# Kernel tuning notes

Measured on AMD Instinct MI355X. Metric: run time of the kernel, lower is better.

Reference implementation:

```python
import jax, jax.numpy as jnp
import numpy as np


def _ens_linear(x, W, b):
    # x: [B,T,Din], W: [E,Din,Dout], b: [E,Dout] -> [E,B,T,Dout]
    return jnp.einsum('btd,edh->ebth', x, W) + b[:, None, None, :]


def _gilr_scan(v, f):
    # h_t = f_t * h_{t-1} + (1 - f_t) * v_t, h_0 = 0 (tie-input-gate linear recurrence)
    def comb(c1, c2):
        a1, b1 = c1
        a2, b2 = c2
        return a2 * a1, a2 * b1 + b2
    _, h = jax.lax.associative_scan(comb, (f, (1.0 - f) * v), axis=1)
    return h


def setup_inputs() -> dict:
    key = jax.random.key(0)
    ks = jax.random.split(key, 7)
    B, T, Din, D = 8, 4096, 512, 512
    x = jax.random.normal(ks[0], (B, T, Din), dtype=jnp.float32)
    s_in = 1.0 / np.sqrt(Din)
    s = 1.0 / np.sqrt(D)
    W_in = jax.random.uniform(ks[1], (2, Din, D), jnp.float32, -s_in, s_in)
    b_in = jax.random.uniform(ks[2], (2, D), jnp.float32, -s_in, s_in)
    W_mid = jax.random.uniform(ks[3], (4, D, D), jnp.float32, -s, s)
    b_mid = jax.random.uniform(ks[4], (4, D), jnp.float32, -s, s)
    W_out = jax.random.uniform(ks[5], (D, D), jnp.float32, -s, s)
    b_out = jax.random.uniform(ks[6], (D,), jnp.float32, -s, s)
    return {"x": x, "W_in": W_in, "b_in": b_in, "W_mid": W_mid,
            "b_mid": b_mid, "W_out": W_out, "b_out": b_out}


def reference(x, W_in, b_in, W_mid, b_mid, W_out, b_out):
    # in_proj (ensemble of 2): u[0] -> v, u[1] -> f
    u = _ens_linear(x, W_in, b_in)
    v = jnp.tanh(u[0])
    f = jax.nn.sigmoid(u[1])
    # first gated linear recurrence (hidden_pre starts at zeros)
    v = _gilr_scan(v, f)
    hidden_pre = v[:, -1:, :]
    # middle_proj (ensemble of 4): f, i, o, z
    u = _ens_linear(v, W_mid, b_mid)
    f2 = jax.nn.sigmoid(u[0])
    i = jax.nn.sigmoid(u[1])
    o = jax.nn.sigmoid(u[2])
    z = jnp.tanh(u[3])
    # second gated linear recurrence (hidden_middle starts at zeros)
    out = _gilr_scan(i * z, f2)
    hidden_middle = out[:, -1:, :]
    out = out * o
    out = out @ W_out + b_out
    hidden = jnp.concatenate((hidden_pre, hidden_middle), axis=-1)
    hidden = jnp.transpose(hidden, (1, 0, 2))  # [1, B, 2D]
    return out, hidden
```

## Files before the change

kernel.cpp:

```cpp
#include <hip/hip_runtime.h>

typedef short short8 __attribute__((ext_vector_type(8)));
typedef float float4v __attribute__((ext_vector_type(4)));
typedef unsigned short u16;
typedef unsigned int u32;

#define T_LEN 4096
#define DDIM 512
#define BATCH 8
#define MROWS 32768
#define CH 32
#define NC 128

__device__ __forceinline__ u16 f2b(float x) {
    unsigned u = __float_as_uint(x);
    unsigned r = (u + 0x7FFFu + ((u >> 16) & 1u)) >> 16;
    return (u16)r;
}
__device__ __forceinline__ float b2f(u16 h) {
    return __uint_as_float((u32)h << 16);
}
__device__ __forceinline__ float sigm(float x) {
    return __builtin_amdgcn_rcpf(1.f + __builtin_amdgcn_exp2f(-1.44269504f * x));
}
__device__ __forceinline__ float tanh_fast(float x) {
    return 1.f - 2.f * __builtin_amdgcn_rcpf(1.f + __builtin_amdgcn_exp2f(2.88539008f * x));
}

__device__ __forceinline__ void gl2lds16(const u16* g, u16* l) {
    __builtin_amdgcn_global_load_lds(
        (const __attribute__((address_space(1))) void*)g,
        (__attribute__((address_space(3))) void*)l, 16, 0, 0);
}

__device__ __forceinline__ void compose_xor(float& A, float& B, int mask,
                                            bool selfIsHi) {
    float pa = __shfl_xor(A, mask);
    float pb = __shfl_xor(B, mask);
    float loA = selfIsHi ? pa : A, loB = selfIsHi ? pb : B;
    float hiA = selfIsHi ? A : pa, hiB = selfIsHi ? B : pb;
    A = hiA * loA;
    B = hiA * loB + hiB;
}

__global__ __launch_bounds__(256) void cvt_x(const float* __restrict__ x,
                                             u16* __restrict__ xb, size_t n) {
    size_t i = ((size_t)blockIdx.x * 256 + threadIdx.x) * 4;
    if (i < n) {
        float4v v = *(const float4v*)&x[i];
        ushort4 p;
        p.x = f2b(v[0]); p.y = f2b(v[1]); p.z = f2b(v[2]); p.w = f2b(v[3]);
        *(ushort4*)&xb[i] = p;
    }
}

template <int MODE>
__global__ __launch_bounds__(256) void cvt_wt(const float* __restrict__ W,
                                              u16* __restrict__ Wt, int N) {
    int idx = blockIdx.x * 256 + threadIdx.x;
    if (idx >= N * 512) return;
    int j = idx >> 9;
    int k = idx & 511;
    int gate, d;
    if (MODE == 1) { gate = (j >> 4) & 1; d = (j >> 5) * 16 + (j & 15); }
    else if (MODE == 2) { gate = (j >> 4) & 3; d = (j >> 6) * 16 + (j & 15); }
    else { gate = 0; d = j; }
    Wt[(size_t)j * 512 + k] = f2b(W[((size_t)gate * 512 + k) * 512 + d]);
}

template <int MODE>
__global__ __launch_bounds__(512, 4) void gemm_act(
    const u16* __restrict__ A, const u16* __restrict__ Bt,
    const float* __restrict__ bias, void* __restrict__ o0v,
    void* __restrict__ o1v, void* __restrict__ o2v,
    float* __restrict__ cA, float* __restrict__ cB) {
    constexpr int K = 512;
    constexpr int BK = 32;
    constexpr int NKT = K / BK;
    constexpr int LBA = 256 * 32;
    constexpr int LBB = 128 * 32;
    constexpr int GX = (MODE == 1) ? 8 : (MODE == 2) ? 16 : 4;
    constexpr int NWG = 128 * GX;
    __shared__ u16 lsA[3][LBA];
    __shared__ u16 lsB[3][LBB];
    const int tid = threadIdx.x;
    const int lane = tid & 63;
    const int wid = tid >> 6;
    const int wr = wid >> 1;
    const int wc = wid & 1;
    const int l0 = lane & 15, lh = lane >> 4;

    const int h = blockIdx.x;
    const int l = (h & 7) * (NWG / 8) + (h >> 3);
    const int bn0 = (l & (GX - 1)) * 128;
    const int bm0 = (l / GX) * 256;

    float4v acc[4][4];
#pragma unroll
    for (int m = 0; m < 4; ++m)
#pragma unroll
        for (int n = 0; n < 4; ++n) acc[m][n] = (float4v){0.f, 0.f, 0.f, 0.f};

    int growA[2], gchA[2], growB, gchB;
#pragma unroll
    for (int i = 0; i < 2; ++i) {
        int flat = i * 512 + tid;
        growA[i] = flat >> 2;
        gchA[i] = (((flat & 3) ^ ((growA[i] >> 1) & 3))) * 8;
    }
    growB = tid >> 2;
    gchB = (((tid & 3) ^ ((growB >> 1) & 3))) * 8;

#define STAGE(buf, kt)                                                        \
    {                                                                         \
        const int k0 = (kt) * BK;                                             \
        _Pragma("unroll") for (int i = 0; i < 2; ++i)                         \
            gl2lds16(&A[(size_t)(bm0 + growA[i]) * K + k0 + gchA[i]],         \
                     &lsA[buf][(i * 512 + tid) * 8]);                         \
        gl2lds16(&Bt[(size_t)(bn0 + growB) * K + k0 + gchB],                  \
                 &lsB[buf][tid * 8]);                                         \
    }

    STAGE(0, 0);
    STAGE(1, 1);

    for (int kt = 0; kt < NKT; ++kt) {
        const int cur = kt % 3;
        if (kt + 1 < NKT)
            asm volatile("s_waitcnt vmcnt(3)" ::: "memory");
        else
            asm volatile("s_waitcnt vmcnt(0)" ::: "memory");
        __builtin_amdgcn_s_barrier();
        __builtin_amdgcn_sched_barrier(0);
        if (kt + 2 < NKT) STAGE((kt + 2) % 3, kt + 2);
        short8 af[4], bf[4];
#pragma unroll
        for (int m = 0; m < 4; ++m) {
            int r = wr * 64 + m * 16 + l0;
            af[m] = *(const short8*)&lsA[cur][r * 32 + ((lh ^ ((r >> 1) & 3)) * 8)];
        }
#pragma unroll
        for (int n = 0; n < 4; ++n) {
            int r = wc * 64 + n * 16 + l0;
            bf[n] = *(const short8*)&lsB[cur][r * 32 + ((lh ^ ((r >> 1) & 3)) * 8)];
        }
        asm volatile("s_waitcnt lgkmcnt(0)" ::: "memory");
        __builtin_amdgcn_sched_barrier(0);
        __builtin_amdgcn_s_setprio(1);
#pragma unroll
        for (int m = 0; m < 4; ++m)
#pragma unroll
            for (int n = 0; n < 4; ++n)
                acc[m][n] = __builtin_amdgcn_mfma_f32_16x16x32_bf16(
                    af[m], bf[n], acc[m][n], 0, 0, 0);
        __builtin_amdgcn_s_setprio(0);
    }
#undef STAGE

    if (MODE == 3) {
#pragma unroll
        for (int m = 0; m < 4; ++m) {
#pragma unroll
            for (int n = 0; n < 4; ++n) {
                int col = bn0 + wc * 64 + n * 16 + l0;
                float bv = bias[col];
#pragma unroll
                for (int r = 0; r < 4; ++r) {
                    int rw = bm0 + wr * 64 + m * 16 + lh * 4 + r;
                    ((float*)o0v)[(size_t)rw * 512 + col] = acc[m][n][r] + bv;
                }
            }
        }
        return;
    }

    const int bb = bm0 >> 12;
    const int tq = (bm0 & 4095) + wr * 64;

    if (MODE == 1) {
        const int base5 = (bn0 + wc * 64) >> 5;
#pragma unroll
        for (int p = 0; p < 2; ++p) {
            const int d = (base5 + p) * 16 + l0;
            const float bvv = bias[d], bvf = bias[512 + d];
            float segA[4], segB[4];
#pragma unroll
            for (int m = 0; m < 4; ++m) {
                float Ap = 1.f, Bp = 0.f;
#pragma unroll
                for (int r = 0; r < 4; ++r) {
                    int rw = bm0 + wr * 64 + m * 16 + lh * 4 + r;
                    float f1 = sigm(acc[m][2 * p + 1][r] + bvf);
                    float g = (1.f - f1) * tanh_fast(acc[m][2 * p][r] + bvv);
                    size_t oidx = (size_t)rw * 512 + d;
                    ((u16*)o0v)[oidx] = f2b(f1);
                    ((u16*)o1v)[oidx] = f2b(g);
                    Bp = f1 * Bp + g;
                    Ap *= f1;
                }
                segA[m] = Ap; segB[m] = Bp;
            }
#pragma unroll
            for (int m = 0; m < 4; ++m) {
                compose_xor(segA[m], segB[m], 16, (lh & 1) != 0);
                compose_xor(segA[m], segB[m], 32, (lh & 2) != 0);
            }
            if (lh == 0) {
                float c0A = segA[1] * segA[0], c0B = segA[1] * segB[0] + segB[1];
                float c1A = segA[3] * segA[2], c1B = segA[3] * segB[2] + segB[3];
                int c0 = tq >> 5;
                size_t ci0 = (size_t)c0 * 4096 + bb * 512 + d;
                size_t ci1 = ci0 + 4096;
                cA[ci0] = c0A; cB[ci0] = c0B;
                cA[ci1] = c1A; cB[ci1] = c1B;
            }
        }
    } else {
        const int d = ((bn0 + wc * 64) >> 6) * 16 + l0;
        const float bv0 = bias[d], bv1 = bias[512 + d];
        const float bv2 = bias[1024 + d], bv3 = bias[1536 + d];
        float segA[4], segB[4];
#pragma unroll
        for (int m = 0; m < 4; ++m) {
            float Ap = 1.f, Bp = 0.f;
#pragma unroll
            for (int r = 0; r < 4; ++r) {
                int rw = bm0 + wr * 64 + m * 16 + lh * 4 + r;
                float f2 = sigm(acc[m][0][r] + bv0);
                float ii = sigm(acc[m][1][r] + bv1);
                float oo = sigm(acc[m][2][r] + bv2);
                float zz = tanh_fast(acc[m][3][r] + bv3);
                float g = (1.f - f2) * ii * zz;
                size_t oidx = (size_t)rw * 512 + d;
                ((u16*)o0v)[oidx] = f2b(f2);
                ((u16*)o1v)[oidx] = f2b(g);
                ((u16*)o2v)[oidx] = f2b(oo);
                Bp = f2 * Bp + g;
                Ap *= f2;
            }
            segA[m] = Ap; segB[m] = Bp;
        }
#pragma unroll
        for (int m = 0; m < 4; ++m) {
            compose_xor(segA[m], segB[m], 16, (lh & 1) != 0);
            compose_xor(segA[m], segB[m], 32, (lh & 2) != 0);
        }
        if (lh == 0) {
            float c0A = segA[1] * segA[0], c0B = segA[1] * segB[0] + segB[1];
            float c1A = segA[3] * segA[2], c1B = segA[3] * segB[2] + segB[3];
            int c0 = tq >> 5;
            size_t ci0 = (size_t)c0 * 4096 + bb * 512 + d;
            size_t ci1 = ci0 + 4096;
            cA[ci0] = c0A; cB[ci0] = c0B;
            cA[ci1] = c1A; cB[ci1] = c1B;
        }
    }
}

__global__ __launch_bounds__(256) void scan_p2(float* __restrict__ cA,
                                               const float* __restrict__ cB) {
    int ln = blockIdx.x * 256 + threadIdx.x;
    float h = 0.f;
    for (int c = 0; c < NC; ++c) {
        size_t ix = (size_t)c * 4096 + ln;
        float a = cA[ix], bb = cB[ix];
        cA[ix] = h;
        h = a * h + bb;
    }
}

template <int S>
__global__ __launch_bounds__(128) void scan_p3(
    const u16* __restrict__ f, const u16* __restrict__ g,
    const u16* __restrict__ o, const float* __restrict__ cA,
    u16* __restrict__ hb, float* __restrict__ hid) {
    int d0 = threadIdx.x * 4;
    int c = blockIdx.x & (NC - 1);
    int b = blockIdx.x >> 7;
    size_t base = ((size_t)b * T_LEN + c * CH) * DDIM + d0;
    size_t ci = (size_t)c * 4096 + b * DDIM + d0;
    float h[4] = {cA[ci], cA[ci + 1], cA[ci + 2], cA[ci + 3]};
    for (int t = 0; t < CH; ++t) {
        ushort4 fq = *(const ushort4*)&f[base];
        ushort4 gq = *(const ushort4*)&g[base];
        float ff[4] = {b2f(fq.x), b2f(fq.y), b2f(fq.z), b2f(fq.w)};
        float gg[4] = {b2f(gq.x), b2f(gq.y), b2f(gq.z), b2f(gq.w)};
        float w[4];
#pragma unroll
        for (int j = 0; j < 4; ++j) {
            h[j] = ff[j] * h[j] + gg[j];
            w[j] = h[j];
        }
        if (S == 2) {
            ushort4 oq = *(const ushort4*)&o[base];
            w[0] *= b2f(oq.x); w[1] *= b2f(oq.y);
            w[2] *= b2f(oq.z); w[3] *= b2f(oq.w);
        }
        ushort4 p;
        p.x = f2b(w[0]); p.y = f2b(w[1]); p.z = f2b(w[2]); p.w = f2b(w[3]);
        *(ushort4*)&hb[base] = p;
        base += DDIM;
    }
    if (c == NC - 1) {
#pragma unroll
        for (int j = 0; j < 4; ++j)
            hid[b * 1024 + (S == 1 ? 0 : 512) + d0 + j] = h[j];
    }
}

extern "C" void kernel_launch(void* const* d_in, const int* in_sizes, int n_in,
                              void* d_out, int out_size, void* d_ws,
                              size_t ws_size, hipStream_t stream) {
    const float* x = (const float*)d_in[0];
    const float* W_in = (const float*)d_in[1];
    const float* b_in = (const float*)d_in[2];
    const float* W_mid = (const float*)d_in[3];
    const float* b_mid = (const float*)d_in[4];
    const float* W_out = (const float*)d_in[5];
    const float* b_out = (const float*)d_in[6];
    float* out = (float*)d_out;
    char* ws = (char*)d_ws;

    const size_t MB = 1u << 20;
    const size_t MD = (size_t)MROWS * DDIM;

    u16* wt_in = (u16*)(ws);
    u16* wt_mid = (u16*)(ws + 1 * MB);
    u16* wt_out = (u16*)(ws + 3 * MB);
    u16* hb = (u16*)(ws + 4 * MB);
    u16* S0 = (u16*)(ws + 36 * MB);
    u16* S1 = (u16*)(ws + 68 * MB);
    u16* S2 = (u16*)(ws + 100 * MB);
    float* cA = (float*)(ws + 164 * MB);
    float* cB = (float*)(ws + 166 * MB);
    float* hid = out + MD;

    cvt_x<<<(int)(MD / 4 / 256), 256, 0, stream>>>(x, hb, MD);
    cvt_wt<1><<<(1024 * 512) / 256, 256, 0, stream>>>(W_in, wt_in, 1024);
    cvt_wt<2><<<(2048 * 512) / 256, 256, 0, stream>>>(W_mid, wt_mid, 2048);
    cvt_wt<3><<<(512 * 512) / 256, 256, 0, stream>>>(W_out, wt_out, 512);

    gemm_act<1><<<1024, 512, 0, stream>>>(hb, wt_in, b_in, S0, S1, nullptr,
                                          cA, cB);
    scan_p2<<<16, 256, 0, stream>>>(cA, cB);
    scan_p3<1><<<1024, 128, 0, stream>>>(S0, S1, nullptr, cA, hb, hid);

    gemm_act<2><<<2048, 512, 0, stream>>>(hb, wt_mid, b_mid, S0, S1, S2,
                                          cA, cB);
    scan_p2<<<16, 256, 0, stream>>>(cA, cB);
    scan_p3<2><<<1024, 128, 0, stream>>>(S0, S1, S2, cA, hb, hid);

    gemm_act<3><<<512, 512, 0, stream>>>(hb, wt_out, b_out, out, nullptr,
                                         nullptr, nullptr, nullptr);
}
```

Before: 244.0 us.

## Fuse fp32-to-bf16 input conversion into first GEMM and merge weight conversions

Removes the standalone cvt_x pass. The first GEMM now reads fp32 x directly, converts it to bf16 in registers and writes it into swizzled LDS, using a double-buffered register-prefetch pipeline with __syncthreads. The three weight-conversion launches are merged into one kernel. This saves a full read/write pass over x and two launches, but the MODE 1 GEMM drops its async global_load_lds triple buffering for a simpler sync-based loop, which may reduce overlap.

```diff
diff --git a/kernel.cpp b/kernel.cpp
--- a/kernel.cpp
+++ b/kernel.cpp
@@ -2,6 +2,7 @@
 
 typedef short short8 __attribute__((ext_vector_type(8)));
 typedef float float4v __attribute__((ext_vector_type(4)));
+typedef int int4v __attribute__((ext_vector_type(4)));
 typedef unsigned short u16;
 typedef unsigned int u32;
 
@@ -16,6 +17,9 @@
     unsigned u = __float_as_uint(x);
     unsigned r = (u + 0x7FFFu + ((u >> 16) & 1u)) >> 16;
     return (u16)r;
+}
+__device__ __forceinline__ u32 pk2(float a, float b) {
+    return (u32)f2b(a) | ((u32)f2b(b) << 16);
 }
 __device__ __forceinline__ float b2f(u16 h) {
     return __uint_as_float((u32)h << 16);
@@ -43,34 +47,31 @@
     B = hiA * loB + hiB;
 }
 
-__global__ __launch_bounds__(256) void cvt_x(const float* __restrict__ x,
-                                             u16* __restrict__ xb, size_t n) {
-    size_t i = ((size_t)blockIdx.x * 256 + threadIdx.x) * 4;
-    if (i < n) {
-        float4v v = *(const float4v*)&x[i];
-        ushort4 p;
-        p.x = f2b(v[0]); p.y = f2b(v[1]); p.z = f2b(v[2]); p.w = f2b(v[3]);
-        *(ushort4*)&xb[i] = p;
-    }
-}
-
-template <int MODE>
-__global__ __launch_bounds__(256) void cvt_wt(const float* __restrict__ W,
-                                              u16* __restrict__ Wt, int N) {
+__global__ __launch_bounds__(256) void cvt_wt_all(
+    const float* __restrict__ W_in, const float* __restrict__ W_mid,
+    const float* __restrict__ W_out, u16* __restrict__ wt_in,
+    u16* __restrict__ wt_mid, u16* __restrict__ wt_out) {
     int idx = blockIdx.x * 256 + threadIdx.x;
-    if (idx >= N * 512) return;
     int j = idx >> 9;
     int k = idx & 511;
-    int gate, d;
-    if (MODE == 1) { gate = (j >> 4) & 1; d = (j >> 5) * 16 + (j & 15); }
-    else if (MODE == 2) { gate = (j >> 4) & 3; d = (j >> 6) * 16 + (j & 15); }
-    else { gate = 0; d = j; }
-    Wt[(size_t)j * 512 + k] = f2b(W[((size_t)gate * 512 + k) * 512 + d]);
+    if (j < 1024) {
+        int gate = (j >> 4) & 1, d = (j >> 5) * 16 + (j & 15);
+        wt_in[(size_t)j * 512 + k] =
+            f2b(W_in[((size_t)gate * 512 + k) * 512 + d]);
+    } else if (j < 3072) {
+        int j2 = j - 1024;
+        int gate = (j2 >> 4) & 3, d = (j2 >> 6) * 16 + (j2 & 15);
+        wt_mid[(size_t)j2 * 512 + k] =
+            f2b(W_mid[((size_t)gate * 512 + k) * 512 + d]);
+    } else {
+        int j3 = j - 3072;
+        wt_out[(size_t)j3 * 512 + k] = f2b(W_out[(size_t)k * 512 + j3]);
+    }
 }
 
 template <int MODE>
 __global__ __launch_bounds__(512, 4) void gemm_act(
-    const u16* __restrict__ A, const u16* __restrict__ Bt,
+    const void* __restrict__ Av, const u16* __restrict__ Bt,
     const float* __restrict__ bias, void* __restrict__ o0v,
     void* __restrict__ o1v, void* __restrict__ o2v,
     float* __restrict__ cA, float* __restrict__ cB) {
@@ -101,15 +102,83 @@
 #pragma unroll
         for (int n = 0; n < 4; ++n) acc[m][n] = (float4v){0.f, 0.f, 0.f, 0.f};
 
-    int growA[2], gchA[2], growB, gchB;
-#pragma unroll
-    for (int i = 0; i < 2; ++i) {
-        int flat = i * 512 + tid;
-        growA[i] = flat >> 2;
-        gchA[i] = (((flat & 3) ^ ((growA[i] >> 1) & 3))) * 8;
-    }
-    growB = tid >> 2;
-    gchB = (((tid & 3) ^ ((growB >> 1) & 3))) * 8;
+    const int growB = tid >> 2;
+    const int gchB = (((tid & 3) ^ ((growB >> 1) & 3))) * 8;
+
+    if constexpr (MODE == 1) {
+        const float* Af = (const float*)Av;
+        const int ar = tid >> 1, ah = tid & 1;
+        const float* agp = &Af[(size_t)(bm0 + ar) * 512 + ah * 16];
+        const int s3 = (ar >> 1) & 3;
+        u16* adst0 = &lsA[0][ar * 32 + (((2 * ah) ^ s3)) * 8];
+        u16* adst1 = &lsA[0][ar * 32 + (((2 * ah + 1) ^ s3)) * 8];
+
+#define CVTWRITE(buf, v0, v1, v2, v3)                                         \
+    {                                                                         \
+        int4v wA = {(int)pk2(v0[0], v0[1]), (int)pk2(v0[2], v0[3]),           \
+                    (int)pk2(v1[0], v1[1]), (int)pk2(v1[2], v1[3])};          \
+        int4v wB = {(int)pk2(v2[0], v2[1]), (int)pk2(v2[2], v2[3]),           \
+                    (int)pk2(v3[0], v3[1]), (int)pk2(v3[2], v3[3])};          \
+        *(int4v*)(adst0 + (buf) * LBA) = wA;                                  \
+        *(int4v*)(adst1 + (buf) * LBA) = wB;                                  \
+    }
+
+        {
+            float4v v0 = *(const float4v*)(agp + 0);
+            float4v v1 = *(const float4v*)(agp + 4);
+            float4v v2 = *(const float4v*)(agp + 8);
+            float4v v3 = *(const float4v*)(agp + 12);
+            gl2lds16(&Bt[(size_t)(bn0 + growB) * K + gchB], &lsB[0][tid * 8]);
+            CVTWRITE(0, v0, v1, v2, v3);
+        }
+        __syncthreads();
+
+        for (int kt = 0; kt < NKT; ++kt) {
+            const int cur = kt & 1, nxt = cur ^ 1;
+            float4v v0, v1, v2, v3;
+            if (kt + 1 < NKT) {
+                const float* ap = agp + (kt + 1) * 32;
+                v0 = *(const float4v*)(ap + 0);
+                v1 = *(const float4v*)(ap + 4);
+                v2 = *(const float4v*)(ap + 8);
+                v3 = *(const float4v*)(ap + 12);
+                gl2lds16(&Bt[(size_t)(bn0 + growB) * K + (kt + 1) * BK + gchB],
+                         &lsB[nxt][tid * 8]);
+            }
+            short8 af[4], bf[4];
+#pragma unroll
+            for (int m = 0; m < 4; ++m) {
+                int r = wr * 64 + m * 16 + l0;
+                af[m] = *(const short8*)&lsA[cur][r * 32 +
+                                                  ((lh ^ ((r >> 1) & 3)) * 8)];
+            }
+#pragma unroll
+            for (int n = 0; n < 4; ++n) {
+                int r = wc * 64 + n * 16 + l0;
+                bf[n] = *(const short8*)&lsB[cur][r * 32 +
+                                                  ((lh ^ ((r >> 1) & 3)) * 8)];
+            }
+            __builtin_amdgcn_s_setprio(1);
+#pragma unroll
+            for (int m = 0; m < 4; ++m)
+#pragma unroll
+                for (int n = 0; n < 4; ++n)
+                    acc[m][n] = __builtin_amdgcn_mfma_f32_16x16x32_bf16(
+                        af[m], bf[n], acc[m][n], 0, 0, 0);
+            __builtin_amdgcn_s_setprio(0);
+            if (kt + 1 < NKT) CVTWRITE(nxt, v0, v1, v2, v3);
+            __syncthreads();
+        }
+#undef CVTWRITE
+    } else {
+        const u16* A = (const u16*)Av;
+        int growA[2], gchA[2];
+#pragma unroll
+        for (int i = 0; i < 2; ++i) {
+            int flat = i * 512 + tid;
+            growA[i] = flat >> 2;
+            gchA[i] = (((flat & 3) ^ ((growA[i] >> 1) & 3))) * 8;
+        }
 
 #define STAGE(buf, kt)                                                        \
     {                                                                         \
@@ -121,41 +190,44 @@
                  &lsB[buf][tid * 8]);                                         \
     }
 
-    STAGE(0, 0);
-    STAGE(1, 1);
-
-    for (int kt = 0; kt < NKT; ++kt) {
-        const int cur = kt % 3;
-        if (kt + 1 < NKT)
-            asm volatile("s_waitcnt vmcnt(3)" ::: "memory");
-        else
-            asm volatile("s_waitcnt vmcnt(0)" ::: "memory");
-        __builtin_amdgcn_s_barrier();
-        __builtin_amdgcn_sched_barrier(0);
-        if (kt + 2 < NKT) STAGE((kt + 2) % 3, kt + 2);
-        short8 af[4], bf[4];
-#pragma unroll
-        for (int m = 0; m < 4; ++m) {
-            int r = wr * 64 + m * 16 + l0;
-            af[m] = *(const short8*)&lsA[cur][r * 32 + ((lh ^ ((r >> 1) & 3)) * 8)];
-        }
-#pragma unroll
-        for (int n = 0; n < 4; ++n) {
-            int r = wc * 64 + n * 16 + l0;
-            bf[n] = *(const short8*)&lsB[cur][r * 32 + ((lh ^ ((r >> 1) & 3)) * 8)];
-        }
-        asm volatile("s_waitcnt lgkmcnt(0)" ::: "memory");
-        __builtin_amdgcn_sched_barrier(0);
-        __builtin_amdgcn_s_setprio(1);
-#pragma unroll
-        for (int m = 0; m < 4; ++m)
-#pragma unroll
-            for (int n = 0; n < 4; ++n)
-                acc[m][n] = __builtin_amdgcn_mfma_f32_16x16x32_bf16(
-                    af[m], bf[n], acc[m][n], 0, 0, 0);
-        __builtin_amdgcn_s_setprio(0);
-    }
+        STAGE(0, 0);
+        STAGE(1, 1);
+
+        for (int kt = 0; kt < NKT; ++kt) {
+            const int cur = kt % 3;
+            if (kt + 1 < NKT)
+                asm volatile("s_waitcnt vmcnt(3)" ::: "memory");
+            else
+                asm volatile("s_waitcnt vmcnt(0)" ::: "memory");
+            __builtin_amdgcn_s_barrier();
+            __builtin_amdgcn_sched_barrier(0);
+            if (kt + 2 < NKT) STAGE((kt + 2) % 3, kt + 2);
+            short8 af[4], bf[4];
+#pragma unroll
+            for (int m = 0; m < 4; ++m) {
+                int r = wr * 64 + m * 16 + l0;
+                af[m] = *(const short8*)&lsA[cur][r * 32 +
+                                                  ((lh ^ ((r >> 1) & 3)) * 8)];
+            }
+#pragma unroll
+            for (int n = 0; n < 4; ++n) {
+                int r = wc * 64 + n * 16 + l0;
+                bf[n] = *(const short8*)&lsB[cur][r * 32 +
+                                                  ((lh ^ ((r >> 1) & 3)) * 8)];
+            }
+            asm volatile("s_waitcnt lgkmcnt(0)" ::: "memory");
+            __builtin_amdgcn_sched_barrier(0);
+            __builtin_amdgcn_s_setprio(1);
+#pragma unroll
+            for (int m = 0; m < 4; ++m)
+#pragma unroll
+                for (int n = 0; n < 4; ++n)
+                    acc[m][n] = __builtin_amdgcn_mfma_f32_16x16x32_bf16(
+                        af[m], bf[n], acc[m][n], 0, 0, 0);
+            __builtin_amdgcn_s_setprio(0);
+        }
 #undef STAGE
+    }
 
     if (MODE == 3) {
 #pragma unroll
@@ -335,12 +407,10 @@
     float* cB = (float*)(ws + 166 * MB);
     float* hid = out + MD;
 
-    cvt_x<<<(int)(MD / 4 / 256), 256, 0, stream>>>(x, hb, MD);
-    cvt_wt<1><<<(1024 * 512) / 256, 256, 0, stream>>>(W_in, wt_in, 1024);
-    cvt_wt<2><<<(2048 * 512) / 256, 256, 0, stream>>>(W_mid, wt_mid, 2048);
-    cvt_wt<3><<<(512 * 512) / 256, 256, 0, stream>>>(W_out, wt_out, 512);
-
-    gemm_act<1><<<1024, 512, 0, stream>>>(hb, wt_in, b_in, S0, S1, nullptr,
+    cvt_wt_all<<<7168, 256, 0, stream>>>(W_in, W_mid, W_out, wt_in, wt_mid,
+                                         wt_out);
+
+    gemm_act<1><<<1024, 512, 0, stream>>>(x, wt_in, b_in, S0, S1, nullptr,
                                           cA, cB);
     scan_p2<<<16, 256, 0, stream>>>(cA, cB);
     scan_p3<1><<<1024, 128, 0, stream>>>(S0, S1, nullptr, cA, hb, hid);
```

After: 265.5 us. 1.09x slower.
